# Kernel optimization log

Measured on AMD Instinct MI355X. Metric: run time of the kernel, lower is better.

Reference implementation:

```python
import jax, jax.numpy as jnp
import numpy as np

N, D, R, E, B = 98304, 128, 3, 491520, 16384


def setup_inputs() -> dict:
    key = jax.random.key(0)
    ks = jax.random.split(key, 12)
    s = 0.05
    return {
        "latents": jax.random.normal(ks[0], (N, D), jnp.float32),
        "Wm": jax.random.normal(ks[1], (R, D, 2 * D), jnp.float32) * s,
        "bm": jax.random.normal(ks[2], (R, D), jnp.float32) * s,
        "W1": jax.random.normal(ks[3], (D, D), jnp.float32) * s,
        "b1": jax.random.normal(ks[4], (D,), jnp.float32) * s,
        "W2": jax.random.normal(ks[5], (D, D), jnp.float32) * s,
        "b2": jax.random.normal(ks[6], (D,), jnp.float32) * s,
        "message_from": jax.random.randint(ks[7], (E,), 0, N),
        "message_to": jax.random.randint(ks[8], (E,), 0, N),
        "view_id": jax.random.randint(ks[9], (N,), 0, B),
        "ch": 6,
        "batch_size": B,
    }


def reference(latents, Wm, bm, W1, b1, W2, b2, message_from, message_to, view_id, ch, batch_size):
    # Message passing rounds: gather -> concat -> Linear+ReLU (dropout=identity in eval) -> scale -> scatter-add
    scale = 1.0 / (ch - 1)
    for r in range(Wm.shape[0]):
        h = jnp.concatenate([latents[message_from], latents[message_to]], axis=-1)  # [E, 2D]
        msg = jax.nn.relu(h @ Wm[r].T + bm[r]) * scale  # [E, D]
        latents = latents.at[message_to].add(msg)
    # Readout: sum latents per sample (note: original's `/ ch` result is discarded, so no division)
    y = jax.ops.segment_sum(latents, view_id, num_segments=batch_size)  # [B, D]
    h = jax.nn.relu(y @ W1.T + b1)
    return h @ W2.T + b2
```

## Files before the change

### kernel.cpp

```cpp
#include <hip/hip_runtime.h>

static constexpr int N  = 98304;
static constexpr int D  = 128;
static constexpr int E  = 491520;
static constexpr int B  = 16384;

using f32x4 = __attribute__((ext_vector_type(4))) float;
using s16x8 = __attribute__((ext_vector_type(8))) short;

typedef __attribute__((address_space(3))) void lds_void;
typedef const __attribute__((address_space(1))) void gbl_void;

__device__ __forceinline__ ushort f2bf(float x) {
    unsigned u = __float_as_uint(x);
    return (ushort)((u + 0x7fffu + ((u >> 16) & 1u)) >> 16);
}
__device__ __forceinline__ float bflo(unsigned u) { return __uint_as_float(u << 16); }
__device__ __forceinline__ float bfhi(unsigned u) { return __uint_as_float(u & 0xffff0000u); }

__global__ void zero2_kernel(int* __restrict__ p) {
    int i = blockIdx.x * 256 + threadIdx.x;
    if (i < N + B) p[i] = 0;
}

__global__ void hist2_kernel(const int* __restrict__ eto, const int* __restrict__ view,
                             int* __restrict__ cnt, int* __restrict__ vcnt) {
    int gid = blockIdx.x * 256 + threadIdx.x;
    if (gid < E) atomicAdd(&cnt[eto[gid]], 1);
    else if (gid < E + N) atomicAdd(&vcnt[view[gid - E]], 1);
}

__global__ __launch_bounds__(256) void scan1_kernel(const int* __restrict__ cnt, int* __restrict__ excl,
                                                    const int* __restrict__ vcnt, int* __restrict__ vexcl,
                                                    int* __restrict__ bsum) {
    __shared__ int s[256];
    const int b = blockIdx.x, t = threadIdx.x;
    const int* src; int* dst; int base;
    if (b < 96) { src = cnt;  dst = excl;  base = b * 1024 + t * 4; }
    else        { src = vcnt; dst = vexcl; base = (b - 96) * 1024 + t * 4; }
    int4 v = *reinterpret_cast<const int4*>(src + base);
    int local = v.x + v.y + v.z + v.w;
    s[t] = local; __syncthreads();
    for (int off = 1; off < 256; off <<= 1) {
        int x = (t >= off) ? s[t - off] : 0;
        __syncthreads();
        s[t] += x;
        __syncthreads();
    }
    int excl_t = s[t] - local;
    if (t == 255) bsum[b] = s[t];
    int4 o;
    o.x = excl_t; o.y = o.x + v.x; o.z = o.y + v.y; o.w = o.z + v.z;
    *reinterpret_cast<int4*>(dst + base) = o;
}

__global__ void scan2_kernel(int* __restrict__ bsum) {
    int t = threadIdx.x;
    if (t == 0) { int run = 0; for (int i = 0;  i < 96;  ++i) { int v = bsum[i]; bsum[i] = run; run += v; } }
    if (t == 1) { int run = 0; for (int i = 96; i < 112; ++i) { int v = bsum[i]; bsum[i] = run; run += v; } }
}

__global__ void scan3_kernel(int* __restrict__ excl, int* __restrict__ vexcl,
                             const int* __restrict__ bsum) {
    int b = blockIdx.x, t = threadIdx.x;
    if (b < 384) { int i = b * 256 + t; excl[i] += bsum[i >> 10]; }
    else         { int i = (b - 384) * 256 + t; vexcl[i] += bsum[96 + (i >> 10)]; }
}

__global__ void scatter2_kernel(const int* __restrict__ efrom, const int* __restrict__ eto,
                                const int* __restrict__ view,
                                int* __restrict__ ecur, int* __restrict__ vcur,
                                int* __restrict__ sfrom, int* __restrict__ perm) {
    int gid = blockIdx.x * 256 + threadIdx.x;
    if (gid < E) {
        int p = atomicAdd(&ecur[eto[gid]], 1);
        sfrom[p] = efrom[gid];
    } else if (gid < E + N) {
        int n = gid - E;
        int p = atomicAdd(&vcur[view[n]], 1);
        perm[p] = n;
    }
}

__global__ void convUV_kernel(const float* __restrict__ Wm, ushort* __restrict__ Wf) {
    int gid = blockIdx.x * 256 + threadIdx.x;
    if (gid >= 3 * 32768) return;
    int r = gid >> 15, rem = gid & 32767;
    int j = rem & 7, lane = (rem >> 3) & 63, grp = rem >> 9;
    int kt = grp >> 4, nt = grp & 15;
    int n = (nt & 7) * 16 + (lane & 15);
    int k = kt * 32 + (lane >> 4) * 8 + j;
    int col = ((nt >> 3) << 7) + k;
    Wf[gid] = f2bf(Wm[((size_t)r * 128 + n) * 256 + col]);
}

__global__ void convW12_kernel(const float* __restrict__ W1, const float* __restrict__ W2,
                               ushort* __restrict__ Wb12) {
    int gid = blockIdx.x * 256 + threadIdx.x;
    if (gid >= 2 * 16384) return;
    int w = gid >> 14, rem = gid & 16383;
    int n = rem >> 7, k = rem & 127;
    int kt = k >> 5, nt = n >> 4;
    int lane = (n & 15) + (((k >> 3) & 3) << 4);
    int j = k & 7;
    const float* W = w ? W2 : W1;
    Wb12[w * 16384 + ((kt * 8 + nt) * 64 + lane) * 8 + j] = f2bf(W[rem]);
}

__global__ __launch_bounds__(512) void uv_kernel(
    const float* __restrict__ Asrc, ushort* __restrict__ Z,
    const ushort* __restrict__ Wft, const float* __restrict__ bm_r)
{
    __shared__ alignas(16) ushort wlds[32768];
    const int t = threadIdx.x;

    #pragma unroll
    for (int it = 0; it < 8; ++it) {
        int idx = t + it * 512;
        __builtin_amdgcn_global_load_lds((gbl_void*)(Wft + idx * 8),
                                         (lds_void*)(wlds + idx * 8), 16, 0, 0);
    }

    const int wave = t >> 6, lane = t & 63;
    const int col16 = lane & 15, kq = lane >> 4;
    const int arow = blockIdx.x * 128 + wave * 16 + col16;

    const float4* Ar = reinterpret_cast<const float4*>(Asrc + (size_t)arow * 128);
    float4 areg[8];
    #pragma unroll
    for (int kt = 0; kt < 4; ++kt) {
        areg[2 * kt]     = Ar[kt * 8 + kq * 2];
        areg[2 * kt + 1] = Ar[kt * 8 + kq * 2 + 1];
    }

    f32x4 acc[16];
    #pragma unroll
    for (int nt = 0; nt < 16; ++nt) acc[nt] = (f32x4){0.f, 0.f, 0.f, 0.f};

    __syncthreads();

    const char* wb = reinterpret_cast<const char*>(wlds);
    #pragma unroll
    for (int kt = 0; kt < 4; ++kt) {
        float4 a0 = areg[2 * kt], a1 = areg[2 * kt + 1];
        union { s16x8 v; ushort u[8]; } pk;
        pk.u[0] = f2bf(a0.x); pk.u[1] = f2bf(a0.y); pk.u[2] = f2bf(a0.z); pk.u[3] = f2bf(a0.w);
        pk.u[4] = f2bf(a1.x); pk.u[5] = f2bf(a1.y); pk.u[6] = f2bf(a1.z); pk.u[7] = f2bf(a1.w);
        #pragma unroll
        for (int nt = 0; nt < 16; ++nt) {
            s16x8 bfr = *reinterpret_cast<const s16x8*>(wb + (((kt * 16 + nt) * 64 + lane) << 4));
            acc[nt] = __builtin_amdgcn_mfma_f32_16x16x32_bf16(pk.v, bfr, acc[nt], 0, 0, 0);
        }
    }

    const int rbase = blockIdx.x * 128 + wave * 16 + kq * 4;
    #pragma unroll
    for (int nt = 0; nt < 16; ++nt) {
        float bias = (nt >= 8) ? bm_r[(nt - 8) * 16 + col16] : 0.f;
        int cfull = ((nt >> 3) << 7) + (nt & 7) * 16 + col16;
        #pragma unroll
        for (int j = 0; j < 4; ++j)
            Z[(size_t)(rbase + j) * 256 + cfull] = f2bf(acc[nt][j] + bias);
    }
}

__global__ __launch_bounds__(256) void edge_sum_kernel(
    const ushort* __restrict__ Z, const float* __restrict__ Lsrc, float* __restrict__ Ldst,
    const int* __restrict__ sfrom, const int* __restrict__ ends, const int* __restrict__ ch_ptr)
{
    const int t = threadIdx.x;
    const int wave = t >> 6, lane = t & 63;
    const float scale = 1.0f / (float)(ch_ptr[0] - 1);
    const int v0 = blockIdx.x * 16 + wave * 4;

    int bnd[5];
    bnd[0] = (v0 == 0) ? 0 : ends[v0 - 1];
    #pragma unroll
    for (int i = 0; i < 4; ++i) bnd[i + 1] = ends[v0 + i];
    unsigned vv[4]; float2 lold[4];
    #pragma unroll
    for (int i = 0; i < 4; ++i) {
        vv[i] = *reinterpret_cast<const unsigned*>(Z + (size_t)(v0 + i) * 256 + 128 + lane * 2);
        lold[i] = *reinterpret_cast<const float2*>(Lsrc + (size_t)(v0 + i) * 128 + lane * 2);
    }

    #pragma unroll
    for (int i = 0; i < 4; ++i) {
        const int lo = bnd[i], hi = bnd[i + 1];
        const float vl = bflo(vv[i]), vh = bfhi(vv[i]);
        float a0 = 0.f, a1 = 0.f;
        int e = lo;
        for (; e + 4 <= hi; e += 4) {
            int f0 = sfrom[e], f1 = sfrom[e + 1], f2 = sfrom[e + 2], f3 = sfrom[e + 3];
            unsigned u0 = *reinterpret_cast<const unsigned*>(Z + (size_t)f0 * 256 + lane * 2);
            unsigned u1 = *reinterpret_cast<const unsigned*>(Z + (size_t)f1 * 256 + lane * 2);
            unsigned u2 = *reinterpret_cast<const unsigned*>(Z + (size_t)f2 * 256 + lane * 2);
            unsigned u3 = *reinterpret_cast<const unsigned*>(Z + (size_t)f3 * 256 + lane * 2);
            a0 += fmaxf(bflo(u0) + vl, 0.f) + fmaxf(bflo(u1) + vl, 0.f)
                + fmaxf(bflo(u2) + vl, 0.f) + fmaxf(bflo(u3) + vl, 0.f);
            a1 += fmaxf(bfhi(u0) + vh, 0.f) + fmaxf(bfhi(u1) + vh, 0.f)
                + fmaxf(bfhi(u2) + vh, 0.f) + fmaxf(bfhi(u3) + vh, 0.f);
        }
        for (; e < hi; ++e) {
            int f0 = sfrom[e];
            unsigned u0 = *reinterpret_cast<const unsigned*>(Z + (size_t)f0 * 256 + lane * 2);
            a0 += fmaxf(bflo(u0) + vl, 0.f);
            a1 += fmaxf(bfhi(u0) + vh, 0.f);
        }
        float2 o;
        o.x = lold[i].x + scale * a0;
        o.y = lold[i].y + scale * a1;
        *reinterpret_cast<float2*>(Ldst + (size_t)(v0 + i) * 128 + lane * 2) = o;
    }
}

__global__ __launch_bounds__(256) void segsum_sorted_kernel(
    const float* __restrict__ L, const int* __restrict__ perm,
    const int* __restrict__ vends, float* __restrict__ y)
{
    const int t = threadIdx.x;
    const int wave = t >> 6, lane = t & 63;
    const int v = blockIdx.x * 4 + wave;
    const int lo = (v == 0) ? 0 : vends[v - 1];
    const int hi = vends[v];

    float a0 = 0.f, a1 = 0.f;
    for (int e = lo; e < hi; e += 2) {
        int last = hi - 1;
        int e1 = (e + 1 < hi) ? e + 1 : last;
        float m1 = (e + 1 < hi) ? 1.f : 0.f;
        int n0 = perm[e], n1 = perm[e1];
        float2 x0 = *reinterpret_cast<const float2*>(L + (size_t)n0 * 128 + lane * 2);
        float2 x1 = *reinterpret_cast<const float2*>(L + (size_t)n1 * 128 + lane * 2);
        a0 += x0.x + m1 * x1.x;
        a1 += x0.y + m1 * x1.y;
    }
    float2 o; o.x = a0; o.y = a1;
    *reinterpret_cast<float2*>(y + (size_t)v * 128 + lane * 2) = o;
}

__global__ __launch_bounds__(256) void readout_mfma_kernel(
    const float* __restrict__ y, float* __restrict__ outp,
    const ushort* __restrict__ Wb1, const ushort* __restrict__ Wb2,
    const float* __restrict__ b1, const float* __restrict__ b2)
{
    __shared__ alignas(16) ushort hs[64 * 128];
    const int t = threadIdx.x;
    const int r0 = blockIdx.x * 64;
    char* hbase = reinterpret_cast<char*>(hs);
    const float4* y4 = reinterpret_cast<const float4*>(y);

    #pragma unroll
    for (int it = 0; it < 4; ++it) {
        int c = t + it * 256;
        int e = c >> 4, p = c & 15;
        int g = p ^ (e & 15);
        float4 a = y4[(size_t)(r0 + e) * 32 + g * 2];
        float4 bq = y4[(size_t)(r0 + e) * 32 + g * 2 + 1];
        union { s16x8 v; ushort u[8]; } pk;
        pk.u[0] = f2bf(a.x); pk.u[1] = f2bf(a.y); pk.u[2] = f2bf(a.z); pk.u[3] = f2bf(a.w);
        pk.u[4] = f2bf(bq.x); pk.u[5] = f2bf(bq.y); pk.u[6] = f2bf(bq.z); pk.u[7] = f2bf(bq.w);
        *reinterpret_cast<s16x8*>(hbase + e * 256 + p * 16) = pk.v;
    }
    __syncthreads();

    const int wave = t >> 6, lane = t & 63;
    const int rrow = wave * 16 + (lane & 15);
    const int kq = lane >> 4;
    const int rx = rrow & 15;
    const char* hrow = hbase + rrow * 256;
    const int col16 = lane & 15;

    f32x4 acc[8];
    #pragma unroll
    for (int nt = 0; nt < 8; ++nt) acc[nt] = (f32x4){0.f, 0.f, 0.f, 0.f};
    const s16x8* wf1 = reinterpret_cast<const s16x8*>(Wb1);
    #pragma unroll
    for (int kt = 0; kt < 4; ++kt) {
        int C = kt * 4 + kq;
        s16x8 a = *reinterpret_cast<const s16x8*>(hrow + ((C ^ rx) & 15) * 16);
        #pragma unroll
        for (int nt = 0; nt < 8; ++nt)
            acc[nt] = __builtin_amdgcn_mfma_f32_16x16x32_bf16(a, wf1[(kt * 8 + nt) * 64 + lane], acc[nt], 0, 0, 0);
    }
    __syncthreads();

    #pragma unroll
    for (int nt = 0; nt < 8; ++nt) {
        float bias = b1[nt * 16 + col16];
        #pragma unroll
        for (int j = 0; j < 4; ++j) {
            int r = wave * 16 + (lane >> 4) * 4 + j;
            float h = fmaxf(acc[nt][j] + bias, 0.f);
            int colfull = nt * 16 + col16;
            int chunk = colfull >> 3;
            int bo = ((chunk ^ (r & 15)) * 16) + (colfull & 7) * 2;
            *reinterpret_cast<ushort*>(hbase + r * 256 + bo) = f2bf(h);
        }
    }
    __syncthreads();

    f32x4 acc2[8];
    #pragma unroll
    for (int nt = 0; nt < 8; ++nt) acc2[nt] = (f32x4){0.f, 0.f, 0.f, 0.f};
    const s16x8* wf2 = reinterpret_cast<const s16x8*>(Wb2);
    #pragma unroll
    for (int kt = 0; kt < 4; ++kt) {
        int C = kt * 4 + kq;
        s16x8 a = *reinterpret_cast<const s16x8*>(hrow + ((C ^ rx) & 15) * 16);
        #pragma unroll
        for (int nt = 0; nt < 8; ++nt)
            acc2[nt] = __builtin_amdgcn_mfma_f32_16x16x32_bf16(a, wf2[(kt * 8 + nt) * 64 + lane], acc2[nt], 0, 0, 0);
    }

    #pragma unroll
    for (int nt = 0; nt < 8; ++nt) {
        float bias = b2[nt * 16 + col16];
        #pragma unroll
        for (int j = 0; j < 4; ++j) {
            int r = r0 + wave * 16 + (lane >> 4) * 4 + j;
            outp[(size_t)r * 128 + nt * 16 + col16] = acc2[nt][j] + bias;
        }
    }
}

extern "C" void kernel_launch(void* const* d_in, const int* in_sizes, int n_in,
                              void* d_out, int out_size, void* d_ws, size_t ws_size,
                              hipStream_t stream) {
    const float* latents = (const float*)d_in[0];
    const float* Wm      = (const float*)d_in[1];
    const float* bm      = (const float*)d_in[2];
    const float* W1      = (const float*)d_in[3];
    const float* b1      = (const float*)d_in[4];
    const float* W2      = (const float*)d_in[5];
    const float* b2      = (const float*)d_in[6];
    const int*   efrom   = (const int*)d_in[7];
    const int*   eto     = (const int*)d_in[8];
    const int*   view    = (const int*)d_in[9];
    const int*   ch      = (const int*)d_in[10];

    float*  L  = (float*)d_ws;
    ushort* Z  = (ushort*)(L + (size_t)N * D);
    float*  yb = (float*)Z;
    ushort* Wb12 = (ushort*)((char*)Z + 8388608);

    char* ob = (char*)d_out;
    ushort* WUVf = (ushort*)ob;
    int* cnt   = (int*)(ob + 196608);
    int* vcnt  = cnt + N;
    int* excl  = vcnt + B;
    int* vexcl = excl + N;
    int* bsum  = vexcl + B;
    int* sfrom = bsum + 128;
    int* perm  = sfrom + E;
    float* outp = (float*)d_out;

    convUV_kernel<<<384, 256, 0, stream>>>(Wm, WUVf);
    zero2_kernel<<<(N + B) / 256, 256, 0, stream>>>(cnt);
    hist2_kernel<<<(E + N) / 256, 256, 0, stream>>>(eto, view, cnt, vcnt);
    scan1_kernel<<<112, 256, 0, stream>>>(cnt, excl, vcnt, vexcl, bsum);
    scan2_kernel<<<1, 64, 0, stream>>>(bsum);
    scan3_kernel<<<448, 256, 0, stream>>>(excl, vexcl, bsum);
    scatter2_kernel<<<(E + N) / 256, 256, 0, stream>>>(efrom, eto, view, excl, vexcl, sfrom, perm);

    uv_kernel<<<N / 128, 512, 0, stream>>>(latents, Z, WUVf, bm);
    edge_sum_kernel<<<N / 16, 256, 0, stream>>>(Z, latents, L, sfrom, excl, ch);
    uv_kernel<<<N / 128, 512, 0, stream>>>(L, Z, WUVf + 32768, bm + D);
    edge_sum_kernel<<<N / 16, 256, 0, stream>>>(Z, L, L, sfrom, excl, ch);
    uv_kernel<<<N / 128, 512, 0, stream>>>(L, Z, WUVf + 65536, bm + 2 * D);
    edge_sum_kernel<<<N / 16, 256, 0, stream>>>(Z, L, L, sfrom, excl, ch);

    convW12_kernel<<<128, 256, 0, stream>>>(W1, W2, Wb12);
    segsum_sorted_kernel<<<B / 4, 256, 0, stream>>>(L, perm, vexcl, yb);
    readout_mfma_kernel<<<B / 64, 256, 0, stream>>>(yb, outp, Wb12, Wb12 + 16384, b1, b2);
}
```

Measured before the change: 283.1 us.

## Batch edge gathers, transpose MFMA output for vector stores, parallelize block scan

The edge-sum kernel now prefetches the first eight neighbor indices and Z rows for all four vertices of a wave in one batch, using clamped indices and masked accumulation, then handles any remaining edges in a tail loop. This raises memory-level parallelism on the latency-bound gather. The uv kernel swaps the MFMA operands so each lane holds four consecutive columns, allowing packed 8-byte stores with a float4 bias load instead of scalar bf16 stores. The single-thread serial scan over block sums is replaced by a 128-thread shared-memory scan. The cost is more registers in edge_sum and some wasted loads for low-degree vertices.

```diff
diff --git a/kernel.cpp b/kernel.cpp
--- a/kernel.cpp
+++ b/kernel.cpp
@@ -54,10 +54,24 @@
     *reinterpret_cast<int4*>(dst + base) = o;
 }
 
-__global__ void scan2_kernel(int* __restrict__ bsum) {
-    int t = threadIdx.x;
-    if (t == 0) { int run = 0; for (int i = 0;  i < 96;  ++i) { int v = bsum[i]; bsum[i] = run; run += v; } }
-    if (t == 1) { int run = 0; for (int i = 96; i < 112; ++i) { int v = bsum[i]; bsum[i] = run; run += v; } }
+__global__ __launch_bounds__(128) void scan2_kernel(int* __restrict__ bsum) {
+    __shared__ int s[128];
+    const int t = threadIdx.x;
+    int val = (t < 112) ? bsum[t] : 0;
+    s[t] = val;
+    __syncthreads();
+    #pragma unroll
+    for (int off = 1; off < 128; off <<= 1) {
+        int x = (t >= off) ? s[t - off] : 0;
+        __syncthreads();
+        s[t] += x;
+        __syncthreads();
+    }
+    int incl = s[t];
+    int seg0_total = s[95];
+    int excl = incl - val;
+    if (t < 96) bsum[t] = excl;
+    else if (t < 112) bsum[t] = excl - seg0_total;
 }
 
 __global__ void scan3_kernel(int* __restrict__ excl, int* __restrict__ vexcl,
@@ -148,19 +162,24 @@
         pk.u[4] = f2bf(a1.x); pk.u[5] = f2bf(a1.y); pk.u[6] = f2bf(a1.z); pk.u[7] = f2bf(a1.w);
         #pragma unroll
         for (int nt = 0; nt < 16; ++nt) {
-            s16x8 bfr = *reinterpret_cast<const s16x8*>(wb + (((kt * 16 + nt) * 64 + lane) << 4));
-            acc[nt] = __builtin_amdgcn_mfma_f32_16x16x32_bf16(pk.v, bfr, acc[nt], 0, 0, 0);
-        }
-    }
-
-    const int rbase = blockIdx.x * 128 + wave * 16 + kq * 4;
+            s16x8 wfr = *reinterpret_cast<const s16x8*>(wb + (((kt * 16 + nt) * 64 + lane) << 4));
+            acc[nt] = __builtin_amdgcn_mfma_f32_16x16x32_bf16(wfr, pk.v, acc[nt], 0, 0, 0);
+        }
+    }
+
+    ushort* zr = Z + (size_t)arow * 256;
     #pragma unroll
     for (int nt = 0; nt < 16; ++nt) {
-        float bias = (nt >= 8) ? bm_r[(nt - 8) * 16 + col16] : 0.f;
-        int cfull = ((nt >> 3) << 7) + (nt & 7) * 16 + col16;
-        #pragma unroll
-        for (int j = 0; j < 4; ++j)
-            Z[(size_t)(rbase + j) * 256 + cfull] = f2bf(acc[nt][j] + bias);
+        float4 bq;
+        if (nt >= 8) bq = *reinterpret_cast<const float4*>(bm_r + (nt - 8) * 16 + kq * 4);
+        else         bq = (float4){0.f, 0.f, 0.f, 0.f};
+        union { uint2 d; ushort u[4]; } pk4;
+        pk4.u[0] = f2bf(acc[nt][0] + bq.x);
+        pk4.u[1] = f2bf(acc[nt][1] + bq.y);
+        pk4.u[2] = f2bf(acc[nt][2] + bq.z);
+        pk4.u[3] = f2bf(acc[nt][3] + bq.w);
+        int cbase = ((nt >> 3) << 7) + (nt & 7) * 16 + kq * 4;
+        *reinterpret_cast<uint2*>(zr + cbase) = pk4.d;
     }
 }
 
@@ -177,6 +196,7 @@
     bnd[0] = (v0 == 0) ? 0 : ends[v0 - 1];
     #pragma unroll
     for (int i = 0; i < 4; ++i) bnd[i + 1] = ends[v0 + i];
+
     unsigned vv[4]; float2 lold[4];
     #pragma unroll
     for (int i = 0; i < 4; ++i) {
@@ -184,32 +204,58 @@
         lold[i] = *reinterpret_cast<const float2*>(Lsrc + (size_t)(v0 + i) * 128 + lane * 2);
     }
 
-    #pragma unroll
-    for (int i = 0; i < 4; ++i) {
-        const int lo = bnd[i], hi = bnd[i + 1];
+    const int cmax = bnd[4] - 1;
+
+    int idx[4][8];
+    #pragma unroll
+    for (int i = 0; i < 4; ++i) {
+        #pragma unroll
+        for (int k = 0; k < 8; ++k) {
+            int c = bnd[i] + k;
+            c = (c > cmax) ? cmax : c;
+            c = (c < 0) ? 0 : c;
+            idx[i][k] = sfrom[c];
+        }
+    }
+
+    unsigned u[4][8];
+    #pragma unroll
+    for (int i = 0; i < 4; ++i) {
+        #pragma unroll
+        for (int k = 0; k < 8; ++k)
+            u[i][k] = *reinterpret_cast<const unsigned*>(Z + (size_t)idx[i][k] * 256 + lane * 2);
+    }
+
+    float A0[4], A1[4];
+    #pragma unroll
+    for (int i = 0; i < 4; ++i) { A0[i] = 0.f; A1[i] = 0.f; }
+    #pragma unroll
+    for (int i = 0; i < 4; ++i) {
         const float vl = bflo(vv[i]), vh = bfhi(vv[i]);
-        float a0 = 0.f, a1 = 0.f;
-        int e = lo;
-        for (; e + 4 <= hi; e += 4) {
-            int f0 = sfrom[e], f1 = sfrom[e + 1], f2 = sfrom[e + 2], f3 = sfrom[e + 3];
-            unsigned u0 = *reinterpret_cast<const unsigned*>(Z + (size_t)f0 * 256 + lane * 2);
-            unsigned u1 = *reinterpret_cast<const unsigned*>(Z + (size_t)f1 * 256 + lane * 2);
-            unsigned u2 = *reinterpret_cast<const unsigned*>(Z + (size_t)f2 * 256 + lane * 2);
-            unsigned u3 = *reinterpret_cast<const unsigned*>(Z + (size_t)f3 * 256 + lane * 2);
-            a0 += fmaxf(bflo(u0) + vl, 0.f) + fmaxf(bflo(u1) + vl, 0.f)
-                + fmaxf(bflo(u2) + vl, 0.f) + fmaxf(bflo(u3) + vl, 0.f);
-            a1 += fmaxf(bfhi(u0) + vh, 0.f) + fmaxf(bfhi(u1) + vh, 0.f)
-                + fmaxf(bfhi(u2) + vh, 0.f) + fmaxf(bfhi(u3) + vh, 0.f);
-        }
-        for (; e < hi; ++e) {
-            int f0 = sfrom[e];
-            unsigned u0 = *reinterpret_cast<const unsigned*>(Z + (size_t)f0 * 256 + lane * 2);
-            a0 += fmaxf(bflo(u0) + vl, 0.f);
-            a1 += fmaxf(bfhi(u0) + vh, 0.f);
-        }
+        #pragma unroll
+        for (int k = 0; k < 8; ++k) {
+            float m = (bnd[i] + k < bnd[i + 1]) ? 1.f : 0.f;
+            A0[i] += m * fmaxf(bflo(u[i][k]) + vl, 0.f);
+            A1[i] += m * fmaxf(bfhi(u[i][k]) + vh, 0.f);
+        }
+    }
+
+    #pragma unroll
+    for (int i = 0; i < 4; ++i) {
+        const float vl = bflo(vv[i]), vh = bfhi(vv[i]);
+        for (int e = bnd[i] + 8; e < bnd[i + 1]; ++e) {
+            int f = sfrom[e];
+            unsigned uu = *reinterpret_cast<const unsigned*>(Z + (size_t)f * 256 + lane * 2);
+            A0[i] += fmaxf(bflo(uu) + vl, 0.f);
+            A1[i] += fmaxf(bfhi(uu) + vh, 0.f);
+        }
+    }
+
+    #pragma unroll
+    for (int i = 0; i < 4; ++i) {
         float2 o;
-        o.x = lold[i].x + scale * a0;
-        o.y = lold[i].y + scale * a1;
+        o.x = lold[i].x + scale * A0[i];
+        o.y = lold[i].y + scale * A1[i];
         *reinterpret_cast<float2*>(Ldst + (size_t)(v0 + i) * 128 + lane * 2) = o;
     }
 }
@@ -359,7 +405,7 @@
     zero2_kernel<<<(N + B) / 256, 256, 0, stream>>>(cnt);
     hist2_kernel<<<(E + N) / 256, 256, 0, stream>>>(eto, view, cnt, vcnt);
     scan1_kernel<<<112, 256, 0, stream>>>(cnt, excl, vcnt, vexcl, bsum);
-    scan2_kernel<<<1, 64, 0, stream>>>(bsum);
+    scan2_kernel<<<1, 128, 0, stream>>>(bsum);
     scan3_kernel<<<448, 256, 0, stream>>>(excl, vexcl, bsum);
     scatter2_kernel<<<(E + N) / 256, 256, 0, stream>>>(efrom, eto, view, excl, vexcl, sfrom, perm);
 
```

Result: slower. 303.4 us (+7.1%).
